# Kernel tuning notes

Measured on AMD Instinct MI355X. Metric: run time of the kernel, lower is better.

## Reference

```python
import jax, jax.numpy as jnp
import numpy as np

C_GAMMA = 0.99   # config.c_gamma
EPS = 0.01       # clamp epsilon in _get_codebook
N_DEVICE = 1.0   # vq_spec.n_device
N_BLOCK = 1.0    # vq_spec.n_block_per_update

B, H, L, D, S = 4, 8, 4096, 128, 1024


def setup_inputs() -> dict:
    key = jax.random.key(0)
    k1, k2 = jax.random.split(key)
    vecs = jax.random.normal(k1, (B, H, L, D), dtype=jnp.float32)
    c_sum = jax.random.normal(k2, (H, S, D), dtype=jnp.float32)
    c_count = jnp.ones((H, S), dtype=jnp.float32)
    loss_mask = jnp.ones((B, L), dtype=jnp.int32)
    return {"vecs": vecs, "c_sum": c_sum, "c_count": c_count, "loss_mask": loss_mask}


def _vq_forward(vecs, c_sum, c_count, loss_mask):
    h, s, d = c_sum.shape
    # codebook (detached, as in _get_codebook)
    c = jax.lax.stop_gradient(c_sum / jnp.clip(c_count, EPS, None)[..., None])  # [H,S,d]

    # get_shortcodes: squared-distance cdist + argmin
    v_sq = jnp.sum(vecs * vecs, axis=-1, keepdims=True)                # [B,H,L,1]
    c_sq = jnp.sum(c * c, axis=-1)                                     # [H,S]
    dots = jnp.einsum('bhlk,hsk->bhls', vecs, c)                       # dense GEMM
    diffs2 = v_sq - 2.0 * dots + c_sq[None, :, None, :]                # [B,H,L,S]
    z = jnp.argmin(diffs2, axis=-1)                                    # [B,H,L] int
    errs2 = jax.nn.relu(jnp.min(diffs2, axis=-1))                      # [B,H,L]

    # get_codewords: gather by shortcode index
    cz = c[jnp.arange(h)[None, :, None], z]                            # [B,H,L,d]

    # straight-through estimator
    vecs_hat = vecs + jax.lax.stop_gradient(cz - vecs)

    mask = loss_mask.astype(vecs.dtype)                                # [B,L]
    n_tok = jnp.maximum(jnp.sum(mask), 1.0)

    # commitment loss: masked mean of quantization errors over tokens and heads
    l_commit = jnp.sum(mask[:, None, :] * errs2) / (h * n_tok)

    # codebook EMA targets via scatter-add (equivalent to one-hot einsum, no [B,H,L,S] one-hot)
    masked_vecs = jax.lax.stop_gradient(vecs * mask[:, None, :, None])
    flat_idx = (jnp.arange(h)[None, :, None] * s + z).reshape(-1)      # [B*H*L]
    c_sum_hat = jax.ops.segment_sum(
        masked_vecs.reshape(-1, d), flat_idx, num_segments=h * s).reshape(h, s, d)
    c_count_hat = jax.ops.segment_sum(
        jnp.broadcast_to(mask[:, None, :], z.shape).reshape(-1), flat_idx,
        num_segments=h * s).reshape(h, s)
    c_sum_hat = N_DEVICE * N_BLOCK * c_sum_hat
    c_count_hat = N_DEVICE * N_BLOCK * c_count_hat

    c_sum_tgt = (1.0 - C_GAMMA) * c_sum_hat + C_GAMMA * c_sum
    c_count_tgt = (1.0 - C_GAMMA) * c_count_hat + C_GAMMA * c_count
    l_codebook = (jnp.sum(jax.lax.stop_gradient(c_sum - c_sum_tgt) * c_sum)
                  + jnp.sum(jax.lax.stop_gradient(c_count - c_count_tgt) * c_count))

    return vecs_hat, z, l_commit, l_codebook


def reference(vecs, c_sum, c_count, loss_mask):
    return _vq_forward(vecs, c_sum, c_count, loss_mask)
```

## Files before the change

kernel.cpp:

```cpp
#include <hip/hip_runtime.h>
#include <hip/hip_bf16.h>

typedef __attribute__((ext_vector_type(8))) short short8;
typedef __attribute__((ext_vector_type(4))) float f32x4;

namespace {
constexpr int B_ = 4, H_ = 8, L_ = 4096, D_ = 128, S_ = 1024;
constexpr int NTOK = B_ * H_ * L_;
constexpr int SCAN_BLK = 256;
constexpr int SCAN_TPW = 32, SCAN_TPB = 128;
constexpr int SCAN_GRID = NTOK / SCAN_TPB;
constexpr int NCHUNK = 32;
constexpr int RES_TPB = 128;
constexpr int RES_GRID = NTOK / RES_TPB;
constexpr int PREP_GRID = H_ * S_ / 16;

constexpr size_t WS_CHI   = 0;
constexpr size_t WS_CLO   = WS_CHI + 2ull * H_ * S_ * D_;
constexpr size_t WS_BN    = WS_CLO + 2ull * H_ * S_ * D_;
constexpr size_t WS_INV   = WS_BN + 4ull * H_ * S_;
constexpr size_t WS_BQ    = WS_INV + 4ull * H_ * S_;
constexpr size_t WS_CAND  = WS_BQ + 4ull * H_ * S_;
constexpr size_t WS_PREPP = WS_CAND + 4ull * NTOK;
constexpr size_t WS_RESC  = WS_PREPP + 8ull * PREP_GRID;
constexpr size_t WS_REST  = WS_RESC + 8ull * RES_GRID;
constexpr size_t WS_RESM  = WS_REST + 8ull * RES_GRID;
}

__device__ inline unsigned short bf_hi(float x) {
    __hip_bfloat16 h = __float2bfloat16(x);
    unsigned short u; __builtin_memcpy(&u, &h, 2); return u;
}
__device__ inline float bf_f(unsigned short u) {
    __hip_bfloat16 h; __builtin_memcpy(&h, &u, 2); return __bfloat162float(h);
}

__global__ __launch_bounds__(256) void vq_prep(
    const float* __restrict__ c_sum, const float* __restrict__ c_count,
    unsigned short* __restrict__ c_hi, unsigned short* __restrict__ c_lo,
    float* __restrict__ Bn, float* __restrict__ inv, float* __restrict__ Bq,
    double* __restrict__ prepPart) {
    const int tid = threadIdx.x;
    const int g = tid >> 4, j = tid & 15;
    const int row = blockIdx.x * 16 + g;
    const int h = row >> 10, s = row & 1023;
    const int st = s >> 4, colp = s & 15;

    float cnt = c_count[row];
    float iv = 1.0f / fmaxf(cnt, 0.01f);
    const float4* src = reinterpret_cast<const float4*>(c_sum + (size_t)row * D_) + 2 * j;
    float4 q0 = src[0], q1 = src[1];
    float e[8] = {q0.x, q0.y, q0.z, q0.w, q1.x, q1.y, q1.z, q1.w};
    short8 h8, l8;
    float sqn = 0.f, sqr = 0.f;
#pragma unroll
    for (int i = 0; i < 8; ++i) {
        float c = e[i] * iv;
        unsigned short hu = bf_hi(c);
        unsigned short lu = bf_hi(c - bf_f(hu));
        h8[i] = (short)hu; l8[i] = (short)lu;
        sqn += c * c; sqr += e[i] * e[i];
    }
    size_t base = (size_t)(h * 64 + st) * 2048 + (j >> 2) * 512 + ((j & 3) * 16 + colp) * 8;
    *reinterpret_cast<short8*>(c_hi + base) = h8;
    *reinterpret_cast<short8*>(c_lo + base) = l8;
#pragma unroll
    for (int o = 8; o; o >>= 1) { sqn += __shfl_xor(sqn, o); sqr += __shfl_xor(sqr, o); }

    __shared__ double sP[16];
    if (j == 0) {
        Bn[row] = sqn; inv[row] = iv; Bq[row] = iv * iv * sqr;
        sP[g] = (double)sqr + (double)cnt * (double)cnt;
    }
    __syncthreads();
    if (tid == 0) {
        double t = 0.0;
#pragma unroll
        for (int i = 0; i < 16; ++i) t += sP[i];
        prepPart[blockIdx.x] = t;
    }
}

#define MFMA(a, b, c) __builtin_amdgcn_mfma_f32_16x16x32_bf16(a, b, c, 0, 0, 0)

__global__ __launch_bounds__(SCAN_BLK) void vq_scan(
    const float* __restrict__ vecs,
    const unsigned short* __restrict__ c_hi, const unsigned short* __restrict__ c_lo,
    const float* __restrict__ Bn, unsigned int* __restrict__ cand) {
    const int tid = threadIdx.x;
    const int wave = tid >> 6, lane = tid & 63;
    const int col = lane & 15, kg = lane >> 4;
    const int blk = ((blockIdx.x & 7) << 7) | (blockIdx.x >> 3);
    const int t0b = blk * SCAN_TPB;
    const int h = (t0b >> 12) & 7;
    const int t0w = t0b + wave * SCAN_TPW;

    __shared__ short sB[2][2][4096];

    short8 ah[2][4], al[2][4];
#pragma unroll
    for (int mt = 0; mt < 2; ++mt)
#pragma unroll
        for (int ck = 0; ck < 4; ++ck) {
            const float* vp = vecs + (size_t)(t0w + mt * 16 + col) * D_ + ck * 32 + kg * 8;
            float4 q0 = *reinterpret_cast<const float4*>(vp);
            float4 q1 = *reinterpret_cast<const float4*>(vp + 4);
            float f[8] = {q0.x, q0.y, q0.z, q0.w, q1.x, q1.y, q1.z, q1.w};
            short8 h8, l8;
#pragma unroll
            for (int i = 0; i < 8; ++i) {
                unsigned short hu = bf_hi(f[i]);
                unsigned short lu = bf_hi(f[i] - bf_f(hu));
                h8[i] = (short)hu; l8[i] = (short)lu;
            }
            ah[mt][ck] = h8; al[mt][ck] = l8;
        }

    const float* Bnh = Bn + h * S_;
    const float4* ghi = reinterpret_cast<const float4*>(c_hi) + (size_t)h * 16384;
    const float4* glo = reinterpret_cast<const float4*>(c_lo) + (size_t)h * 16384;

    float4 sg0 = ghi[tid], sg1 = ghi[256 + tid], sg2 = glo[tid], sg3 = glo[256 + tid];
    {
        float4* pH = reinterpret_cast<float4*>(&sB[0][0][0]);
        float4* pL = reinterpret_cast<float4*>(&sB[0][1][0]);
        pH[tid] = sg0; pH[256 + tid] = sg1;
        pL[tid] = sg2; pL[256 + tid] = sg3;
    }
    __syncthreads();

    float m1[2][4], m2[2][4];
#pragma unroll
    for (int mt = 0; mt < 2; ++mt)
#pragma unroll
        for (int i = 0; i < 4; ++i) { m1[mt][i] = INFINITY; m2[mt][i] = INFINITY; }

#pragma unroll 1
    for (int c = 0; c < NCHUNK; ++c) {
        const int cur = c & 1, nxt = cur ^ 1;
        if (c + 1 < NCHUNK) {
            const float4* gh = ghi + (size_t)(c + 1) * 512;
            const float4* gl = glo + (size_t)(c + 1) * 512;
            sg0 = gh[tid]; sg1 = gh[256 + tid]; sg2 = gl[tid]; sg3 = gl[256 + tid];
        }
#pragma unroll
        for (int tl = 0; tl < 2; ++tl) {
            const int st = c * 2 + tl;
            short8 bh[4], bl[4];
#pragma unroll
            for (int ck = 0; ck < 4; ++ck) {
                bh[ck] = *reinterpret_cast<const short8*>(&sB[cur][0][tl * 2048 + ck * 512 + lane * 8]);
                bl[ck] = *reinterpret_cast<const short8*>(&sB[cur][1][tl * 2048 + ck * 512 + lane * 8]);
            }
            f32x4 pa0 = {0.f,0.f,0.f,0.f}, pb0 = {0.f,0.f,0.f,0.f}, pc0 = {0.f,0.f,0.f,0.f};
            f32x4 pa1 = {0.f,0.f,0.f,0.f}, pb1 = {0.f,0.f,0.f,0.f}, pc1 = {0.f,0.f,0.f,0.f};
#pragma unroll
            for (int ck = 0; ck < 4; ++ck) {
                pa0 = MFMA(ah[0][ck], bh[ck], pa0);
                pa1 = MFMA(ah[1][ck], bh[ck], pa1);
                pb0 = MFMA(ah[0][ck], bl[ck], pb0);
                pb1 = MFMA(ah[1][ck], bl[ck], pb1);
                pc0 = MFMA(al[0][ck], bh[ck], pc0);
                pc1 = MFMA(al[1][ck], bh[ck], pc1);
            }
            const float bsc = Bnh[st * 16 + col];
#pragma unroll
            for (int i = 0; i < 4; ++i) {
                float d = fmaf(pa0[i] + pb0[i] + pc0[i], -2.f, bsc);
                float pk = __uint_as_float((__float_as_uint(d) & 0xFFFFFFC0u) | (unsigned)st);
                bool cc = pk < m1[0][i];
                m2[0][i] = cc ? m1[0][i] : fminf(pk, m2[0][i]);
                m1[0][i] = cc ? pk : m1[0][i];
                d = fmaf(pa1[i] + pb1[i] + pc1[i], -2.f, bsc);
                pk = __uint_as_float((__float_as_uint(d) & 0xFFFFFFC0u) | (unsigned)st);
                cc = pk < m1[1][i];
                m2[1][i] = cc ? m1[1][i] : fminf(pk, m2[1][i]);
                m1[1][i] = cc ? pk : m1[1][i];
            }
        }
        if (c + 1 < NCHUNK) {
            float4* pH = reinterpret_cast<float4*>(&sB[nxt][0][0]);
            float4* pL = reinterpret_cast<float4*>(&sB[nxt][1][0]);
            pH[tid] = sg0; pH[256 + tid] = sg1;
            pL[tid] = sg2; pL[256 + tid] = sg3;
        }
        __syncthreads();
    }

#pragma unroll
    for (int mt = 0; mt < 2; ++mt)
#pragma unroll
        for (int i = 0; i < 4; ++i) {
            float a1v = m1[mt][i], a2v = m2[mt][i];
            int x1 = (int)((__float_as_uint(a1v) & 63u) << 4) | col;
            int x2 = (int)((__float_as_uint(a2v) & 63u) << 4) | col;
#pragma unroll
            for (int mask = 1; mask < 16; mask <<= 1) {
                float b1 = __shfl_xor(a1v, mask), b2 = __shfl_xor(a2v, mask);
                int y1 = __shfl_xor(x1, mask), y2 = __shfl_xor(x2, mask);
                bool sw = (b1 < a1v) || (b1 == a1v && y1 < x1);
                float w1 = sw ? b1 : a1v; int wi1 = sw ? y1 : x1;
                float r  = sw ? a1v : b1; int ri  = sw ? x1 : y1;
                float w2 = sw ? b2 : a2v; int wi2 = sw ? y2 : x2;
                bool s2 = (r < w2) || (r == w2 && ri < wi2);
                a1v = w1; x1 = wi1;
                a2v = s2 ? r : w2; x2 = s2 ? ri : wi2;
            }
            if (col == 0) {
                int lt = mt * 16 + kg * 4 + i;
                cand[t0w + lt] = (unsigned)x1 | ((unsigned)x2 << 10);
            }
        }
}

__global__ __launch_bounds__(256) void vq_rescore(
    const float* __restrict__ vecs, const float* __restrict__ c_sum,
    const float* __restrict__ c_count, const int* __restrict__ lmask,
    const float* __restrict__ inv_a, const float* __restrict__ Bq,
    const unsigned int* __restrict__ cand,
    double* __restrict__ resC, double* __restrict__ resT,
    long long* __restrict__ resM,
    float* __restrict__ out_hat, float* __restrict__ out_z) {
    const int tid = threadIdx.x;
    const int lane = tid & 63;
    const int g = tid >> 4, j = tid & 15;
    const int blk = ((blockIdx.x & 7) << 7) | (blockIdx.x >> 3);
    const int t0 = blk * RES_TPB;
    const int h = (t0 >> 12) & 7;
    const int b = t0 >> 15;

    __shared__ float sDot[RES_TPB][2];
    __shared__ float sVs[RES_TPB];
    __shared__ int sZ[RES_TPB];
    __shared__ double sC[4], sT[4];
    __shared__ long long sM[4];

#pragma unroll 1
    for (int r = 0; r < 16; ++r) {
        const int p = r * 16 + g;
        const int lt = p >> 1, slot = p & 1;
        const unsigned int cw = cand[t0 + lt];
        const int cidx = slot ? (int)((cw >> 10) & 1023u) : (int)(cw & 1023u);
        const float4* vp = reinterpret_cast<const float4*>(vecs + (size_t)(t0 + lt) * D_);
        const float4* cp = reinterpret_cast<const float4*>(c_sum + ((size_t)h * S_ + cidx) * D_);
        float4 qa = vp[j], qb = vp[16 + j];
        float4 pa = cp[j], pb = cp[16 + j];
        float dot = qa.x * pa.x + qa.y * pa.y + qa.z * pa.z + qa.w * pa.w
                  + qb.x * pb.x + qb.y * pb.y + qb.z * pb.z + qb.w * pb.w;
        float vs = qa.x * qa.x + qa.y * qa.y + qa.z * qa.z + qa.w * qa.w
                 + qb.x * qb.x + qb.y * qb.y + qb.z * qb.z + qb.w * qb.w;
#pragma unroll
        for (int o = 8; o; o >>= 1) { dot += __shfl_xor(dot, o); vs += __shfl_xor(vs, o); }
        if (j == 0) {
            sDot[lt][slot] = dot;
            if (slot == 0) sVs[lt] = vs;
        }
    }
    __syncthreads();

    double commit = 0.0, tokc = 0.0;
    long long mcnt = 0;
    if (tid < RES_TPB) {
        const int lt = tid, tok = t0 + lt;
        const unsigned int cw = cand[tok];
        const int c0 = (int)(cw & 1023u), c1 = (int)((cw >> 10) & 1023u);
        const float dot0 = sDot[lt][0], dot1 = sDot[lt][1], vs = sVs[lt];
        const float dist0 = vs - 2.f * (inv_a[h * S_ + c0] * dot0) + Bq[h * S_ + c0];
        const float dist1 = vs - 2.f * (inv_a[h * S_ + c1] * dot1) + Bq[h * S_ + c1];
        const bool w0 = (dist0 < dist1) || (dist0 == dist1 && c0 < c1);
        const float dwin = w0 ? dist0 : dist1;
        const int zwin = w0 ? c0 : c1;
        const float dotw = w0 ? dot0 : dot1;
        out_z[tok] = (float)zwin;
        sZ[lt] = zwin;
        const int lm = lmask[b * L_ + (tok & (L_ - 1))];
        const float mask = (float)lm;
        commit = (double)(mask * fmaxf(dwin, 0.f));
        tokc = (double)mask * ((double)dotw + (double)c_count[h * S_ + zwin]);
        if (h == 0) mcnt = lm;
    }
#pragma unroll
    for (int o = 32; o; o >>= 1) {
        commit += __shfl_down(commit, o);
        tokc   += __shfl_down(tokc, o);
        mcnt   += __shfl_down(mcnt, o);
    }
    const int w = tid >> 6;
    if (lane == 0) { sC[w] = commit; sT[w] = tokc; sM[w] = mcnt; }
    __syncthreads();
    if (tid == 0) {
        resC[blockIdx.x] = sC[0] + sC[1] + sC[2] + sC[3];
        resT[blockIdx.x] = sT[0] + sT[1] + sT[2] + sT[3];
        resM[blockIdx.x] = sM[0] + sM[1] + sM[2] + sM[3];
    }

    const int hw = tid >> 5, hl = tid & 31;
#pragma unroll
    for (int r0 = 0; r0 < 16; ++r0) {
        int r = r0 * 8 + hw;
        int z = sZ[r];
        float ivz = inv_a[h * S_ + z];
        float4 p = reinterpret_cast<const float4*>(c_sum + ((size_t)h * S_ + z) * D_)[hl];
        float4 o; o.x = p.x * ivz; o.y = p.y * ivz; o.z = p.z * ivz; o.w = p.w * ivz;
        reinterpret_cast<float4*>(out_hat + (size_t)(t0 + r) * D_)[hl] = o;
    }
}

__global__ __launch_bounds__(256) void vq_final(
    const double* __restrict__ prepPart, const double* __restrict__ resC,
    const double* __restrict__ resT, const long long* __restrict__ resM,
    float* __restrict__ out_sc) {
    const int tid = threadIdx.x;
    double cs = 0.0, cm = 0.0, tk = 0.0;
    long long mk = 0;
    for (int i = tid; i < PREP_GRID; i += 256) cs += prepPart[i];
    for (int i = tid; i < RES_GRID; i += 256) { cm += resC[i]; tk += resT[i]; mk += resM[i]; }
    __shared__ double aC[4], aM[4], aT[4];
    __shared__ long long aK[4];
#pragma unroll
    for (int o = 32; o; o >>= 1) {
        cs += __shfl_down(cs, o);
        cm += __shfl_down(cm, o);
        tk += __shfl_down(tk, o);
        mk += __shfl_down(mk, o);
    }
    const int w = tid >> 6;
    if ((tid & 63) == 0) { aC[w] = cs; aM[w] = cm; aT[w] = tk; aK[w] = mk; }
    __syncthreads();
    if (tid == 0) {
        double CS = aC[0] + aC[1] + aC[2] + aC[3];
        double CM = aM[0] + aM[1] + aM[2] + aM[3];
        double TK = aT[0] + aT[1] + aT[2] + aT[3];
        double NT = (double)(aK[0] + aK[1] + aK[2] + aK[3]);
        if (NT < 1.0) NT = 1.0;
        out_sc[0] = (float)(CM / ((double)H_ * NT));
        out_sc[1] = (float)(0.01 * (CS - TK));
    }
}

extern "C" void kernel_launch(void* const* d_in, const int* in_sizes, int n_in,
                              void* d_out, int out_size, void* d_ws, size_t ws_size,
                              hipStream_t stream) {
    const float* vecs    = (const float*)d_in[0];
    const float* c_sum   = (const float*)d_in[1];
    const float* c_count = (const float*)d_in[2];
    const int*   lmask   = (const int*)d_in[3];

    char* ws = (char*)d_ws;
    unsigned short* c_hi = (unsigned short*)(ws + WS_CHI);
    unsigned short* c_lo = (unsigned short*)(ws + WS_CLO);
    float* Bn  = (float*)(ws + WS_BN);
    float* inv = (float*)(ws + WS_INV);
    float* Bq  = (float*)(ws + WS_BQ);
    unsigned int* cand = (unsigned int*)(ws + WS_CAND);
    double* prepPart = (double*)(ws + WS_PREPP);
    double* resC = (double*)(ws + WS_RESC);
    double* resT = (double*)(ws + WS_REST);
    long long* resM = (long long*)(ws + WS_RESM);

    float* out = (float*)d_out;
    float* out_sc = out + (size_t)out_size - 2;
    float* out_z  = out_sc - (size_t)NTOK;

    vq_prep<<<PREP_GRID, 256, 0, stream>>>(c_sum, c_count, c_hi, c_lo, Bn, inv, Bq, prepPart);
    vq_scan<<<SCAN_GRID, SCAN_BLK, 0, stream>>>(vecs, c_hi, c_lo, Bn, cand);
    vq_rescore<<<RES_GRID, 256, 0, stream>>>(vecs, c_sum, c_count, lmask, inv, Bq,
                                             cand, resC, resT, resM, out, out_z);
    vq_final<<<1, 256, 0, stream>>>(prepPart, resC, resT, resM, out_sc);
}
```

Baseline: 152.6 us.

## Stream codebook tiles via direct global-to-LDS loads with 4-stage ring buffer

The scan kernel now copies codebook hi/lo tiles straight from global memory into shared memory with global_load_lds, using a 4-slot ring that keeps three 16-column tiles in flight. The register-staged double buffer and its 32-chunk loop are gone. The Bn norms are also preloaded into shared memory, and MFMA priority is raised with setprio. The aim is to hide load latency, free VGPRs and drop the register-to-LDS store pass. In exchange it relies on hand-written vmcnt waits and sched barriers, which must stay correct.

```diff
diff --git a/kernel.cpp b/kernel.cpp
--- a/kernel.cpp
+++ b/kernel.cpp
@@ -10,7 +10,6 @@
 constexpr int SCAN_BLK = 256;
 constexpr int SCAN_TPW = 32, SCAN_TPB = 128;
 constexpr int SCAN_GRID = NTOK / SCAN_TPB;
-constexpr int NCHUNK = 32;
 constexpr int RES_TPB = 128;
 constexpr int RES_GRID = NTOK / RES_TPB;
 constexpr int PREP_GRID = H_ * S_ / 16;
@@ -33,6 +32,12 @@
 }
 __device__ inline float bf_f(unsigned short u) {
     __hip_bfloat16 h; __builtin_memcpy(&h, &u, 2); return __bfloat162float(h);
+}
+
+__device__ __forceinline__ void gll16(const void* g, void* l) {
+    __builtin_amdgcn_global_load_lds(
+        (const __attribute__((address_space(1))) unsigned int*)g,
+        (__attribute__((address_space(3))) unsigned int*)l, 16, 0, 0);
 }
 
 __global__ __launch_bounds__(256) void vq_prep(
@@ -95,7 +100,8 @@
     const int h = (t0b >> 12) & 7;
     const int t0w = t0b + wave * SCAN_TPW;
 
-    __shared__ short sB[2][2][4096];
+    __shared__ char sBuf[4 * 8192];
+    __shared__ float sBn[S_];
 
     short8 ah[2][4], al[2][4];
 #pragma unroll
@@ -115,19 +121,23 @@
             }
             ah[mt][ck] = h8; al[mt][ck] = l8;
         }
-
-    const float* Bnh = Bn + h * S_;
-    const float4* ghi = reinterpret_cast<const float4*>(c_hi) + (size_t)h * 16384;
-    const float4* glo = reinterpret_cast<const float4*>(c_lo) + (size_t)h * 16384;
-
-    float4 sg0 = ghi[tid], sg1 = ghi[256 + tid], sg2 = glo[tid], sg3 = glo[256 + tid];
-    {
-        float4* pH = reinterpret_cast<float4*>(&sB[0][0][0]);
-        float4* pL = reinterpret_cast<float4*>(&sB[0][1][0]);
-        pH[tid] = sg0; pH[256 + tid] = sg1;
-        pL[tid] = sg2; pL[256 + tid] = sg3;
-    }
-    __syncthreads();
+    __builtin_amdgcn_sched_barrier(0);
+
+    const char* chB = (const char*)c_hi + (size_t)h * 262144;
+    const char* clB = (const char*)c_lo + (size_t)h * 262144;
+    const char* bnB = (const char*)(Bn + h * S_);
+
+    gll16(bnB + wave * 1024 + lane * 16, (char*)sBn + wave * 1024);
+#pragma unroll
+    for (int t = 0; t < 3; ++t) {
+        char* slot = &sBuf[t * 8192];
+        gll16(chB + (size_t)t * 4096 + wave * 1024 + lane * 16, slot + wave * 1024);
+        gll16(clB + (size_t)t * 4096 + wave * 1024 + lane * 16, slot + 4096 + wave * 1024);
+    }
+    asm volatile("s_waitcnt vmcnt(4)" ::: "memory");
+    __builtin_amdgcn_sched_barrier(0);
+    __builtin_amdgcn_s_barrier();
+    __builtin_amdgcn_sched_barrier(0);
 
     float m1[2][4], m2[2][4];
 #pragma unroll
@@ -136,55 +146,59 @@
         for (int i = 0; i < 4; ++i) { m1[mt][i] = INFINITY; m2[mt][i] = INFINITY; }
 
 #pragma unroll 1
-    for (int c = 0; c < NCHUNK; ++c) {
-        const int cur = c & 1, nxt = cur ^ 1;
-        if (c + 1 < NCHUNK) {
-            const float4* gh = ghi + (size_t)(c + 1) * 512;
-            const float4* gl = glo + (size_t)(c + 1) * 512;
-            sg0 = gh[tid]; sg1 = gh[256 + tid]; sg2 = gl[tid]; sg3 = gl[256 + tid];
-        }
-#pragma unroll
-        for (int tl = 0; tl < 2; ++tl) {
-            const int st = c * 2 + tl;
-            short8 bh[4], bl[4];
-#pragma unroll
-            for (int ck = 0; ck < 4; ++ck) {
-                bh[ck] = *reinterpret_cast<const short8*>(&sB[cur][0][tl * 2048 + ck * 512 + lane * 8]);
-                bl[ck] = *reinterpret_cast<const short8*>(&sB[cur][1][tl * 2048 + ck * 512 + lane * 8]);
-            }
-            f32x4 pa0 = {0.f,0.f,0.f,0.f}, pb0 = {0.f,0.f,0.f,0.f}, pc0 = {0.f,0.f,0.f,0.f};
-            f32x4 pa1 = {0.f,0.f,0.f,0.f}, pb1 = {0.f,0.f,0.f,0.f}, pc1 = {0.f,0.f,0.f,0.f};
-#pragma unroll
-            for (int ck = 0; ck < 4; ++ck) {
-                pa0 = MFMA(ah[0][ck], bh[ck], pa0);
-                pa1 = MFMA(ah[1][ck], bh[ck], pa1);
-                pb0 = MFMA(ah[0][ck], bl[ck], pb0);
-                pb1 = MFMA(ah[1][ck], bl[ck], pb1);
-                pc0 = MFMA(al[0][ck], bh[ck], pc0);
-                pc1 = MFMA(al[1][ck], bh[ck], pc1);
-            }
-            const float bsc = Bnh[st * 16 + col];
-#pragma unroll
-            for (int i = 0; i < 4; ++i) {
-                float d = fmaf(pa0[i] + pb0[i] + pc0[i], -2.f, bsc);
-                float pk = __uint_as_float((__float_as_uint(d) & 0xFFFFFFC0u) | (unsigned)st);
-                bool cc = pk < m1[0][i];
-                m2[0][i] = cc ? m1[0][i] : fminf(pk, m2[0][i]);
-                m1[0][i] = cc ? pk : m1[0][i];
-                d = fmaf(pa1[i] + pb1[i] + pc1[i], -2.f, bsc);
-                pk = __uint_as_float((__float_as_uint(d) & 0xFFFFFFC0u) | (unsigned)st);
-                cc = pk < m1[1][i];
-                m2[1][i] = cc ? m1[1][i] : fminf(pk, m2[1][i]);
-                m1[1][i] = cc ? pk : m1[1][i];
-            }
-        }
-        if (c + 1 < NCHUNK) {
-            float4* pH = reinterpret_cast<float4*>(&sB[nxt][0][0]);
-            float4* pL = reinterpret_cast<float4*>(&sB[nxt][1][0]);
-            pH[tid] = sg0; pH[256 + tid] = sg1;
-            pL[tid] = sg2; pL[256 + tid] = sg3;
-        }
-        __syncthreads();
+    for (int t = 0; t < 64; ++t) {
+        if (t + 3 < 64) {
+            char* slot = &sBuf[((t + 3) & 3) * 8192];
+            gll16(chB + (size_t)(t + 3) * 4096 + wave * 1024 + lane * 16, slot + wave * 1024);
+            gll16(clB + (size_t)(t + 3) * 4096 + wave * 1024 + lane * 16, slot + 4096 + wave * 1024);
+        }
+        __builtin_amdgcn_sched_barrier(0);
+
+        const char* slot = &sBuf[(t & 3) * 8192];
+        short8 bh[4], bl[4];
+#pragma unroll
+        for (int ck = 0; ck < 4; ++ck) {
+            bh[ck] = *reinterpret_cast<const short8*>(slot + ck * 1024 + lane * 16);
+            bl[ck] = *reinterpret_cast<const short8*>(slot + 4096 + ck * 1024 + lane * 16);
+        }
+        asm volatile("s_waitcnt lgkmcnt(0)" ::: "memory");
+        __builtin_amdgcn_sched_barrier(0);
+
+        __builtin_amdgcn_s_setprio(1);
+        f32x4 pa0 = {0.f,0.f,0.f,0.f}, pb0 = {0.f,0.f,0.f,0.f}, pc0 = {0.f,0.f,0.f,0.f};
+        f32x4 pa1 = {0.f,0.f,0.f,0.f}, pb1 = {0.f,0.f,0.f,0.f}, pc1 = {0.f,0.f,0.f,0.f};
+#pragma unroll
+        for (int ck = 0; ck < 4; ++ck) {
+            pa0 = MFMA(ah[0][ck], bh[ck], pa0);
+            pa1 = MFMA(ah[1][ck], bh[ck], pa1);
+            pb0 = MFMA(ah[0][ck], bl[ck], pb0);
+            pb1 = MFMA(ah[1][ck], bl[ck], pb1);
+            pc0 = MFMA(al[0][ck], bh[ck], pc0);
+            pc1 = MFMA(al[1][ck], bh[ck], pc1);
+        }
+        __builtin_amdgcn_s_setprio(0);
+
+        const float bsc = sBn[t * 16 + col];
+#pragma unroll
+        for (int i = 0; i < 4; ++i) {
+            float d = fmaf(pa0[i] + pb0[i] + pc0[i], -2.f, bsc);
+            float pk = __uint_as_float((__float_as_uint(d) & 0xFFFFFFC0u) | (unsigned)t);
+            bool cc = pk < m1[0][i];
+            m2[0][i] = cc ? m1[0][i] : fminf(pk, m2[0][i]);
+            m1[0][i] = cc ? pk : m1[0][i];
+            d = fmaf(pa1[i] + pb1[i] + pc1[i], -2.f, bsc);
+            pk = __uint_as_float((__float_as_uint(d) & 0xFFFFFFC0u) | (unsigned)t);
+            cc = pk < m1[1][i];
+            m2[1][i] = cc ? m1[1][i] : fminf(pk, m2[1][i]);
+            m1[1][i] = cc ? pk : m1[1][i];
+        }
+
+        if (t < 61)      asm volatile("s_waitcnt vmcnt(4)" ::: "memory");
+        else if (t == 61) asm volatile("s_waitcnt vmcnt(2)" ::: "memory");
+        else              asm volatile("s_waitcnt vmcnt(0)" ::: "memory");
+        __builtin_amdgcn_sched_barrier(0);
+        __builtin_amdgcn_s_barrier();
+        __builtin_amdgcn_sched_barrier(0);
     }
 
 #pragma unroll
```

After: 181.2 us. 1.19x slower.

## Switch scan GEMM to 32x32x16 MFMA with folded -2 scale and bias init

Applied to the files above, without the earlier changes.

The distance scan now uses 32x32x16 bf16 MFMA tiles instead of 16x16x32, so each wave covers 32 tokens against 32 codewords per chunk with a single 16-wide accumulator. The -2 factor is folded into the precomputed codebook split, and the accumulator starts at the codeword norm, which removes the per-element fma and the sum of three partial accumulators. The prep kernel's layout is changed to match the new B-fragment ordering, and the top-2 reduction now shuffles across 32 lanes. This trades fewer, larger MFMA issues and less VALU work for a longer dependent MFMA chain on one accumulator, and it changes rounding slightly because -2c is split into hi/lo parts instead of c.

```diff
diff --git a/kernel.cpp b/kernel.cpp
--- a/kernel.cpp
+++ b/kernel.cpp
@@ -2,7 +2,7 @@
 #include <hip/hip_bf16.h>
 
 typedef __attribute__((ext_vector_type(8))) short short8;
-typedef __attribute__((ext_vector_type(4))) float f32x4;
+typedef __attribute__((ext_vector_type(16))) float f32x16;
 
 namespace {
 constexpr int B_ = 4, H_ = 8, L_ = 4096, D_ = 128, S_ = 1024;
@@ -44,7 +44,7 @@
     const int g = tid >> 4, j = tid & 15;
     const int row = blockIdx.x * 16 + g;
     const int h = row >> 10, s = row & 1023;
-    const int st = s >> 4, colp = s & 15;
+    const int st = s >> 5, colp = s & 31;
 
     float cnt = c_count[row];
     float iv = 1.0f / fmaxf(cnt, 0.01f);
@@ -56,12 +56,13 @@
 #pragma unroll
     for (int i = 0; i < 8; ++i) {
         float c = e[i] * iv;
-        unsigned short hu = bf_hi(c);
-        unsigned short lu = bf_hi(c - bf_f(hu));
+        float t = -2.f * c;
+        unsigned short hu = bf_hi(t);
+        unsigned short lu = bf_hi(t - bf_f(hu));
         h8[i] = (short)hu; l8[i] = (short)lu;
         sqn += c * c; sqr += e[i] * e[i];
     }
-    size_t base = (size_t)(h * 64 + st) * 2048 + (j >> 2) * 512 + ((j & 3) * 16 + colp) * 8;
+    size_t base = (size_t)(h * 32 + st) * 4096 + (j >> 1) * 512 + ((j & 1) * 32 + colp) * 8;
     *reinterpret_cast<short8*>(c_hi + base) = h8;
     *reinterpret_cast<short8*>(c_lo + base) = l8;
 #pragma unroll
@@ -81,7 +82,7 @@
     }
 }
 
-#define MFMA(a, b, c) __builtin_amdgcn_mfma_f32_16x16x32_bf16(a, b, c, 0, 0, 0)
+#define MFMA32(a, b, c) __builtin_amdgcn_mfma_f32_32x32x16_bf16(a, b, c, 0, 0, 0)
 
 __global__ __launch_bounds__(SCAN_BLK) void vq_scan(
     const float* __restrict__ vecs,
@@ -89,7 +90,7 @@
     const float* __restrict__ Bn, unsigned int* __restrict__ cand) {
     const int tid = threadIdx.x;
     const int wave = tid >> 6, lane = tid & 63;
-    const int col = lane & 15, kg = lane >> 4;
+    const int col = lane & 31, khalf = lane >> 5;
     const int blk = ((blockIdx.x & 7) << 7) | (blockIdx.x >> 3);
     const int t0b = blk * SCAN_TPB;
     const int h = (t0b >> 12) & 7;
@@ -97,24 +98,22 @@
 
     __shared__ short sB[2][2][4096];
 
-    short8 ah[2][4], al[2][4];
-#pragma unroll
-    for (int mt = 0; mt < 2; ++mt)
-#pragma unroll
-        for (int ck = 0; ck < 4; ++ck) {
-            const float* vp = vecs + (size_t)(t0w + mt * 16 + col) * D_ + ck * 32 + kg * 8;
-            float4 q0 = *reinterpret_cast<const float4*>(vp);
-            float4 q1 = *reinterpret_cast<const float4*>(vp + 4);
-            float f[8] = {q0.x, q0.y, q0.z, q0.w, q1.x, q1.y, q1.z, q1.w};
-            short8 h8, l8;
-#pragma unroll
-            for (int i = 0; i < 8; ++i) {
-                unsigned short hu = bf_hi(f[i]);
-                unsigned short lu = bf_hi(f[i] - bf_f(hu));
-                h8[i] = (short)hu; l8[i] = (short)lu;
-            }
-            ah[mt][ck] = h8; al[mt][ck] = l8;
-        }
+    short8 ah[8], al[8];
+#pragma unroll
+    for (int kc = 0; kc < 8; ++kc) {
+        const float* vp = vecs + (size_t)(t0w + col) * D_ + kc * 16 + khalf * 8;
+        float4 q0 = *reinterpret_cast<const float4*>(vp);
+        float4 q1 = *reinterpret_cast<const float4*>(vp + 4);
+        float f[8] = {q0.x, q0.y, q0.z, q0.w, q1.x, q1.y, q1.z, q1.w};
+        short8 h8, l8;
+#pragma unroll
+        for (int i = 0; i < 8; ++i) {
+            unsigned short hu = bf_hi(f[i]);
+            unsigned short lu = bf_hi(f[i] - bf_f(hu));
+            h8[i] = (short)hu; l8[i] = (short)lu;
+        }
+        ah[kc] = h8; al[kc] = l8;
+    }
 
     const float* Bnh = Bn + h * S_;
     const float4* ghi = reinterpret_cast<const float4*>(c_hi) + (size_t)h * 16384;
@@ -129,54 +128,40 @@
     }
     __syncthreads();
 
-    float m1[2][4], m2[2][4];
-#pragma unroll
-    for (int mt = 0; mt < 2; ++mt)
-#pragma unroll
-        for (int i = 0; i < 4; ++i) { m1[mt][i] = INFINITY; m2[mt][i] = INFINITY; }
+    float m1[16], m2[16];
+#pragma unroll
+    for (int i = 0; i < 16; ++i) { m1[i] = INFINITY; m2[i] = INFINITY; }
 
 #pragma unroll 1
     for (int c = 0; c < NCHUNK; ++c) {
         const int cur = c & 1, nxt = cur ^ 1;
+        const float bsc = Bnh[c * 32 + col];
         if (c + 1 < NCHUNK) {
             const float4* gh = ghi + (size_t)(c + 1) * 512;
             const float4* gl = glo + (size_t)(c + 1) * 512;
             sg0 = gh[tid]; sg1 = gh[256 + tid]; sg2 = gl[tid]; sg3 = gl[256 + tid];
         }
-#pragma unroll
-        for (int tl = 0; tl < 2; ++tl) {
-            const int st = c * 2 + tl;
-            short8 bh[4], bl[4];
-#pragma unroll
-            for (int ck = 0; ck < 4; ++ck) {
-                bh[ck] = *reinterpret_cast<const short8*>(&sB[cur][0][tl * 2048 + ck * 512 + lane * 8]);
-                bl[ck] = *reinterpret_cast<const short8*>(&sB[cur][1][tl * 2048 + ck * 512 + lane * 8]);
-            }
-            f32x4 pa0 = {0.f,0.f,0.f,0.f}, pb0 = {0.f,0.f,0.f,0.f}, pc0 = {0.f,0.f,0.f,0.f};
-            f32x4 pa1 = {0.f,0.f,0.f,0.f}, pb1 = {0.f,0.f,0.f,0.f}, pc1 = {0.f,0.f,0.f,0.f};
-#pragma unroll
-            for (int ck = 0; ck < 4; ++ck) {
-                pa0 = MFMA(ah[0][ck], bh[ck], pa0);
-                pa1 = MFMA(ah[1][ck], bh[ck], pa1);
-                pb0 = MFMA(ah[0][ck], bl[ck], pb0);
-                pb1 = MFMA(ah[1][ck], bl[ck], pb1);
-                pc0 = MFMA(al[0][ck], bh[ck], pc0);
-                pc1 = MFMA(al[1][ck], bh[ck], pc1);
-            }
-            const float bsc = Bnh[st * 16 + col];
-#pragma unroll
-            for (int i = 0; i < 4; ++i) {
-                float d = fmaf(pa0[i] + pb0[i] + pc0[i], -2.f, bsc);
-                float pk = __uint_as_float((__float_as_uint(d) & 0xFFFFFFC0u) | (unsigned)st);
-                bool cc = pk < m1[0][i];
-                m2[0][i] = cc ? m1[0][i] : fminf(pk, m2[0][i]);
-                m1[0][i] = cc ? pk : m1[0][i];
-                d = fmaf(pa1[i] + pb1[i] + pc1[i], -2.f, bsc);
-                pk = __uint_as_float((__float_as_uint(d) & 0xFFFFFFC0u) | (unsigned)st);
-                cc = pk < m1[1][i];
-                m2[1][i] = cc ? m1[1][i] : fminf(pk, m2[1][i]);
-                m1[1][i] = cc ? pk : m1[1][i];
-            }
+        short8 bh[8], bl[8];
+#pragma unroll
+        for (int kc = 0; kc < 8; ++kc) {
+            bh[kc] = *reinterpret_cast<const short8*>(&sB[cur][0][kc * 512 + lane * 8]);
+            bl[kc] = *reinterpret_cast<const short8*>(&sB[cur][1][kc * 512 + lane * 8]);
+        }
+        f32x16 acc;
+#pragma unroll
+        for (int i = 0; i < 16; ++i) acc[i] = bsc;
+#pragma unroll
+        for (int kc = 0; kc < 8; ++kc) acc = MFMA32(ah[kc], bh[kc], acc);
+#pragma unroll
+        for (int kc = 0; kc < 8; ++kc) acc = MFMA32(ah[kc], bl[kc], acc);
+#pragma unroll
+        for (int kc = 0; kc < 8; ++kc) acc = MFMA32(al[kc], bh[kc], acc);
+#pragma unroll
+        for (int i = 0; i < 16; ++i) {
+            float pk = __uint_as_float((__float_as_uint(acc[i]) & 0xFFFFFFC0u) | (unsigned)c);
+            bool cc = pk < m1[i];
+            m2[i] = cc ? m1[i] : fminf(pk, m2[i]);
+            m1[i] = cc ? pk : m1[i];
         }
         if (c + 1 < NCHUNK) {
             float4* pH = reinterpret_cast<float4*>(&sB[nxt][0][0]);
@@ -188,29 +173,27 @@
     }
 
 #pragma unroll
-    for (int mt = 0; mt < 2; ++mt)
-#pragma unroll
-        for (int i = 0; i < 4; ++i) {
-            float a1v = m1[mt][i], a2v = m2[mt][i];
-            int x1 = (int)((__float_as_uint(a1v) & 63u) << 4) | col;
-            int x2 = (int)((__float_as_uint(a2v) & 63u) << 4) | col;
-#pragma unroll
-            for (int mask = 1; mask < 16; mask <<= 1) {
-                float b1 = __shfl_xor(a1v, mask), b2 = __shfl_xor(a2v, mask);
-                int y1 = __shfl_xor(x1, mask), y2 = __shfl_xor(x2, mask);
-                bool sw = (b1 < a1v) || (b1 == a1v && y1 < x1);
-                float w1 = sw ? b1 : a1v; int wi1 = sw ? y1 : x1;
-                float r  = sw ? a1v : b1; int ri  = sw ? x1 : y1;
-                float w2 = sw ? b2 : a2v; int wi2 = sw ? y2 : x2;
-                bool s2 = (r < w2) || (r == w2 && ri < wi2);
-                a1v = w1; x1 = wi1;
-                a2v = s2 ? r : w2; x2 = s2 ? ri : wi2;
-            }
-            if (col == 0) {
-                int lt = mt * 16 + kg * 4 + i;
-                cand[t0w + lt] = (unsigned)x1 | ((unsigned)x2 << 10);
-            }
-        }
+    for (int i = 0; i < 16; ++i) {
+        float a1v = m1[i], a2v = m2[i];
+        int x1 = (int)((__float_as_uint(a1v) & 63u) << 5) | col;
+        int x2 = (int)((__float_as_uint(a2v) & 63u) << 5) | col;
+#pragma unroll
+        for (int mask = 1; mask < 32; mask <<= 1) {
+            float b1 = __shfl_xor(a1v, mask), b2 = __shfl_xor(a2v, mask);
+            int y1 = __shfl_xor(x1, mask), y2 = __shfl_xor(x2, mask);
+            bool sw = (b1 < a1v) || (b1 == a1v && y1 < x1);
+            float w1 = sw ? b1 : a1v; int wi1 = sw ? y1 : x1;
+            float r  = sw ? a1v : b1; int ri  = sw ? x1 : y1;
+            float w2 = sw ? b2 : a2v; int wi2 = sw ? y2 : x2;
+            bool s2 = (r < w2) || (r == w2 && ri < wi2);
+            a1v = w1; x1 = wi1;
+            a2v = s2 ? r : w2; x2 = s2 ? ri : wi2;
+        }
+        if (col == 0) {
+            int rrow = (i & 3) + 8 * (i >> 2) + 4 * khalf;
+            cand[t0w + rrow] = (unsigned)x1 | ((unsigned)x2 << 10);
+        }
+    }
 }
 
 __global__ __launch_bounds__(256) void vq_rescore(
```

Result: slower. 164.5 us (+7.8%).
